# Kernel optimization log

Measured on AMD Instinct MI355X. Metric: run time of the kernel, lower is better.

## Reference

```python
import jax, jax.numpy as jnp
import numpy as np

EPS = 1e-6
NORM_FACTOR = 1000.0  # self.normalization_factor, aggregation 'sum'

# ---- Lorentz manifold (curvature -1, hyperboloid <x,x>_L = -1) ----

def _linner(x, y):
    # Lorentz inner product, keepdim on last axis
    return -x[..., :1] * y[..., :1] + jnp.sum(x[..., 1:] * y[..., 1:], axis=-1, keepdims=True)

def _proj_tan0(u):
    return jnp.concatenate([jnp.zeros_like(u[..., :1]), u[..., 1:]], axis=-1)

def _expmap0(u):
    sp = u[..., 1:]
    n = jnp.sqrt(jnp.clip(jnp.sum(sp * sp, axis=-1, keepdims=True), EPS))
    return jnp.concatenate([jnp.cosh(n), jnp.sinh(n) / n * sp], axis=-1)

def _logmap0(x):
    x0 = jnp.clip(x[..., :1], 1.0 + EPS)
    d = jnp.arccosh(x0)
    sp = x[..., 1:] * (d / jnp.sqrt(x0 * x0 - 1.0))
    return jnp.concatenate([jnp.zeros_like(x0), sp], axis=-1)

def _dist(x, y):
    return jnp.arccosh(jnp.clip(-_linner(x, y), 1.0 + EPS))

def _logmap(x, y):
    alpha = jnp.clip(-_linner(x, y), 1.0 + EPS)
    u = y - alpha * x                      # y + <x,y>_L x
    return jnp.arccosh(alpha) * u / jnp.sqrt(alpha * alpha - 1.0)

def _expmap(x, u):
    n = jnp.sqrt(jnp.clip(_linner(u, u), EPS))
    return jnp.cosh(n) * x + jnp.sinh(n) / n * u

def _proju(x, u):
    return u + _linner(x, u) * x

def _transp0(y, v):
    # parallel transport from origin o=(1,0,...,0) to y
    coef = _linner(y, v) / (1.0 + y[..., :1])
    oy = jnp.concatenate([y[..., :1] + 1.0, y[..., 1:]], axis=-1)
    return v + coef * oy

def _layernorm(x, g, b, eps=1e-5):
    m = jnp.mean(x, axis=-1, keepdims=True)
    v = jnp.mean((x - m) ** 2, axis=-1, keepdims=True)
    return (x - m) / jnp.sqrt(v + eps) * g + b


def setup_inputs() -> dict:
    N, E, D, ED = 10000, 320000, 128, 2
    key = jax.random.key(0)
    ks = jax.random.split(key, 10)
    # nodes on the hyperboloid: expmap0 of a small tangent vector
    h_tan = 0.02 * jax.random.normal(ks[0], (N, D), dtype=jnp.float32)
    h = _expmap0(_proj_tan0(h_tan))
    edge_attr = jax.random.normal(ks[1], (E, ED), dtype=jnp.float32)
    row = jax.random.randint(ks[2], (E,), 0, N, dtype=jnp.int32)
    col = jax.random.randint(ks[3], (E,), 0, N, dtype=jnp.int32)
    node_mask = jnp.ones((N, 1), dtype=jnp.float32)
    edge_mask = jnp.ones((E, 1), dtype=jnp.float32)
    s = 1.0 / np.sqrt(D)
    W = s * jax.random.normal(ks[4], (D, D), dtype=jnp.float32)
    bias = 0.0 * jax.random.normal(ks[5], (1, D), dtype=jnp.float32)  # init.constant_(bias, 0)
    att_in = 2 * D + ED + 1  # x_row, x_col, edge_attr + geodesic
    att_w1 = (1.0 / np.sqrt(att_in)) * jax.random.normal(ks[6], (att_in, D), dtype=jnp.float32)
    att_b1 = jnp.zeros((D,), dtype=jnp.float32)
    att_w2 = s * jax.random.normal(ks[7], (D, 1), dtype=jnp.float32)
    att_b2 = jnp.zeros((1,), dtype=jnp.float32)
    ln_gamma = jnp.ones((D - 1,), dtype=jnp.float32)
    ln_beta = jnp.zeros((D - 1,), dtype=jnp.float32)
    return {"h": h, "edge_attr": edge_attr, "row": row, "col": col,
            "node_mask": node_mask, "edge_mask": edge_mask, "W": W, "bias": bias,
            "att_w1": att_w1, "att_b1": att_b1, "att_w2": att_w2, "att_b2": att_b2,
            "ln_gamma": ln_gamma, "ln_beta": ln_beta}


def reference(h, edge_attr, row, col, node_mask, edge_mask, W, bias,
              att_w1, att_b1, att_w2, att_b2, ln_gamma, ln_beta):
    N = h.shape[0]
    # ---- HypLinear ----
    xt = _logmap0(h) @ W                  # Linear(in,out,bias=False)
    x = _expmap0(_proj_tan0(xt))
    b = _transp0(x, _proj_tan0(bias))
    x = _expmap(x, b)
    # ---- HypAgg ----
    x_tan = _logmap0(x)
    xr, xc = x[row], x[col]
    geo = _dist(xr, xc)                   # [E,1]
    att_in = jnp.concatenate([x_tan[row], x_tan[col], edge_attr, geo], axis=-1)
    hid = jax.nn.silu(att_in @ att_w1 + att_b1)
    att = jax.nn.sigmoid(hid @ att_w2 + att_b2) * edge_mask   # [E,1]
    loc = _logmap(xr, xc)                 # [E,D]
    agg = jax.ops.segment_sum(loc * att, row, num_segments=N) / NORM_FACTOR
    x = _expmap(x, _proju(x, agg))
    # ---- HNorm (Lorentz: LN on spatial components only) ----
    ht = _logmap0(x)
    sp = _layernorm(ht[..., 1:], ln_gamma, ln_beta)
    x = _expmap0(jnp.concatenate([ht[..., :1], sp], axis=-1))
    # ---- HypAct (manifold_out = Lorentz as well) ----
    xt = _proj_tan0(jax.nn.silu(_logmap0(x)))
    return _expmap0(xt)
```

## Files before the change

kernel.cpp:

```cpp
#include <hip/hip_runtime.h>
#include <math.h>

#define D 128
#define NPB 8
#define EPS1 (1.0f + 1e-6f)

__device__ __forceinline__ float sum16(float v) {
#pragma unroll
    for (int o = 8; o; o >>= 1) v += __shfl_xor(v, o, 64);
    return v;
}

__device__ __forceinline__ float facosh(float a) {
    return __logf(a + sqrtf(fmaxf(a * a - 1.0f, 0.0f)));
}

__device__ __forceinline__ void unpack8(const float4& a, const float4& b,
                                        float* d) {
    d[0] = a.x; d[1] = a.y; d[2] = a.z; d[3] = a.w;
    d[4] = b.x; d[5] = b.y; d[6] = b.z; d[7] = b.w;
}

__device__ __forceinline__ void bsum8(float* v, float (*wred)[NPB], int lane,
                                      int wid) {
    __syncthreads();
#pragma unroll
    for (int o = 32; o; o >>= 1)
#pragma unroll
        for (int n = 0; n < NPB; n++) v[n] += __shfl_xor(v[n], o, 64);
    if (lane == 0)
#pragma unroll
        for (int n = 0; n < NPB; n++) wred[wid][n] = v[n];
    __syncthreads();
#pragma unroll
    for (int n = 0; n < NPB; n++) v[n] = wred[0][n] + wred[1][n];
}

__global__ __launch_bounds__(128) void node_pre8(
    const float* __restrict__ h, const float* __restrict__ W,
    const float* __restrict__ bias, const float* __restrict__ att_w1,
    const float* __restrict__ att_b1, float* __restrict__ XQ,
    float* __restrict__ P_out, const int* __restrict__ row,
    int* __restrict__ cnt, int N, int E) {
    int i0 = blockIdx.x * NPB;
    int j = threadIdx.x, lane = j & 63, wid = j >> 6;
    __shared__ __align__(16) float t8[NPB][D];
    __shared__ float wred[2][NPB];

    float hj[NPB];
#pragma unroll
    for (int n = 0; n < NPB; n++) {
        hj[n] = (i0 + n < N) ? h[(size_t)(i0 + n) * D + j] : 0.0f;
        t8[n][j] = hj[n];
    }
    __syncthreads();
    float tj[NPB];
#pragma unroll
    for (int n = 0; n < NPB; n++) {
        float h0 = fmaxf(t8[n][0], EPS1);
        float fac = facosh(h0) * rsqrtf(h0 * h0 - 1.0f);
        tj[n] = (j == 0) ? 0.0f : hj[n] * fac;
    }
    __syncthreads();
#pragma unroll
    for (int n = 0; n < NPB; n++) t8[n][j] = tj[n];
    __syncthreads();

    float xt[NPB];
#pragma unroll
    for (int n = 0; n < NPB; n++) xt[n] = 0.0f;
    for (int k0 = 0; k0 < D; k0 += 4) {
        float w0 = W[(k0 + 0) * D + j], w1 = W[(k0 + 1) * D + j];
        float w2 = W[(k0 + 2) * D + j], w3 = W[(k0 + 3) * D + j];
#pragma unroll
        for (int n = 0; n < NPB; n++) {
            float4 tv = *(const float4*)&t8[n][k0];
            xt[n] = fmaf(tv.x, w0,
                         fmaf(tv.y, w1, fmaf(tv.z, w2, fmaf(tv.w, w3, xt[n]))));
        }
    }
    if (j == 0)
#pragma unroll
        for (int n = 0; n < NPB; n++) xt[n] = 0.0f;

    float v8[NPB];
#pragma unroll
    for (int n = 0; n < NPB; n++) v8[n] = xt[n] * xt[n];
    bsum8(v8, wred, lane, wid);
    float xj[NPB];
#pragma unroll
    for (int n = 0; n < NPB; n++) {
        float nn = sqrtf(fmaxf(v8[n], 1e-6f));
        float e = __expf(nn), ei = __fdividef(1.0f, e);
        float ch = 0.5f * (e + ei), sh = 0.5f * (e - ei);
        xj[n] = (j == 0) ? ch : __fdividef(sh, nn) * xt[n];
    }

    float vj = (j == 0) ? 0.0f : bias[j];
#pragma unroll
    for (int n = 0; n < NPB; n++) v8[n] = xj[n] * vj;
    bsum8(v8, wred, lane, wid);
    __syncthreads();
#pragma unroll
    for (int n = 0; n < NPB; n++) t8[n][j] = xj[n];
    __syncthreads();
    float bj[NPB];
#pragma unroll
    for (int n = 0; n < NPB; n++) {
        float X0 = t8[n][0];
        float coef = __fdividef(v8[n], 1.0f + X0);
        bj[n] = vj + coef * ((j == 0) ? (X0 + 1.0f) : xj[n]);
    }
#pragma unroll
    for (int n = 0; n < NPB; n++)
        v8[n] = (j == 0) ? -bj[n] * bj[n] : bj[n] * bj[n];
    bsum8(v8, wred, lane, wid);
    float xnj[NPB];
#pragma unroll
    for (int n = 0; n < NPB; n++) {
        float nb = sqrtf(fmaxf(v8[n], 1e-6f));
        float e = __expf(nb), ei = __fdividef(1.0f, e);
        float ch = 0.5f * (e + ei), sh = 0.5f * (e - ei);
        xnj[n] = ch * xj[n] + __fdividef(sh, nb) * bj[n];
        if (i0 + n < N) XQ[(size_t)(i0 + n) * 256 + j] = xnj[n];
    }

    __syncthreads();
#pragma unroll
    for (int n = 0; n < NPB; n++) t8[n][j] = xnj[n];
    __syncthreads();
    float xtj[NPB];
#pragma unroll
    for (int n = 0; n < NPB; n++) {
        float Y0 = fmaxf(t8[n][0], EPS1);
        float f = facosh(Y0) * rsqrtf(Y0 * Y0 - 1.0f);
        xtj[n] = (j == 0) ? 0.0f : xnj[n] * f;
    }
    __syncthreads();
#pragma unroll
    for (int n = 0; n < NPB; n++) t8[n][j] = xtj[n];
    __syncthreads();

    float p[NPB], q[NPB];
    float b1 = att_b1[j];
#pragma unroll
    for (int n = 0; n < NPB; n++) {
        p[n] = b1;
        q[n] = 0.0f;
    }
    for (int k0 = 0; k0 < D; k0 += 4) {
        float a0 = att_w1[(k0 + 0) * D + j], a1 = att_w1[(k0 + 1) * D + j];
        float a2 = att_w1[(k0 + 2) * D + j], a3 = att_w1[(k0 + 3) * D + j];
        float c0 = att_w1[(D + k0 + 0) * D + j], c1 = att_w1[(D + k0 + 1) * D + j];
        float c2 = att_w1[(D + k0 + 2) * D + j], c3 = att_w1[(D + k0 + 3) * D + j];
#pragma unroll
        for (int n = 0; n < NPB; n++) {
            float4 tv = *(const float4*)&t8[n][k0];
            p[n] = fmaf(tv.x, a0,
                        fmaf(tv.y, a1, fmaf(tv.z, a2, fmaf(tv.w, a3, p[n]))));
            q[n] = fmaf(tv.x, c0,
                        fmaf(tv.y, c1, fmaf(tv.z, c2, fmaf(tv.w, c3, q[n]))));
        }
    }
#pragma unroll
    for (int n = 0; n < NPB; n++)
        if (i0 + n < N) {
            P_out[(size_t)(i0 + n) * D + j] = p[n];
            XQ[(size_t)(i0 + n) * 256 + 128 + j] = q[n];
        }

    int gtid = blockIdx.x * 128 + threadIdx.x;
    int tot = gridDim.x * 128;
    for (int e2 = gtid; e2 < E; e2 += tot) atomicAdd(&cnt[row[e2]], 1);
}

__global__ __launch_bounds__(1024) void scan_kernel(const int* __restrict__ cnt,
                                                    int* __restrict__ off,
                                                    int* __restrict__ cursor,
                                                    int N) {
    __shared__ int wsum[16];
    __shared__ int carry_s;
    int tid = threadIdx.x, lane = tid & 63, wid = tid >> 6;
    if (tid == 0) carry_s = 0;
    __syncthreads();
    for (int base = 0; base < N; base += 1024) {
        int idx = base + tid;
        int v = (idx < N) ? cnt[idx] : 0;
        int orig = v;
#pragma unroll
        for (int o = 1; o < 64; o <<= 1) {
            int t = __shfl_up(v, o, 64);
            if (lane >= o) v += t;
        }
        if (lane == 63) wsum[wid] = v;
        __syncthreads();
        if (wid == 0 && lane < 16) {
            int w = wsum[lane];
#pragma unroll
            for (int o = 1; o < 16; o <<= 1) {
                int t = __shfl_up(w, o, 64);
                if (lane >= o) w += t;
            }
            wsum[lane] = w;
        }
        __syncthreads();
        int carry = carry_s;
        int wbase = (wid == 0) ? 0 : wsum[wid - 1];
        int excl = carry + wbase + v - orig;
        if (idx < N) {
            off[idx] = excl;
            cursor[idx] = excl;
        }
        __syncthreads();
        if (tid == 1023) carry_s = carry + wsum[15];
        __syncthreads();
    }
}

__global__ void scatter_kernel(const int* __restrict__ row,
                               const int* __restrict__ col,
                               const float* __restrict__ edge_attr,
                               const float* __restrict__ edge_mask,
                               int* __restrict__ cursor,
                               float4* __restrict__ rec, int E) {
    const float2* ea2 = (const float2*)edge_attr;
    for (int e = blockIdx.x * blockDim.x + threadIdx.x; e < E;
         e += gridDim.x * blockDim.x) {
        int r = row[e];
        int pos = atomicAdd(&cursor[r], 1);
        float2 a = ea2[e];
        rec[pos] = make_float4(__int_as_float(col[e]), a.x, a.y, edge_mask[e]);
    }
}

__global__ __launch_bounds__(256) void edge_agg(
    const float* __restrict__ XQ, const float* __restrict__ P,
    const float4* __restrict__ rec, const int* __restrict__ off,
    const int* __restrict__ cnt, const float* __restrict__ w1c,
    const float* __restrict__ att_w2, const float* __restrict__ att_b2,
    float* __restrict__ agg, int N) {
    int tid = threadIdx.x, lane = tid & 63;
    int sub = lane & 15, grp = lane >> 4;
    int i = blockIdx.x * 4 + (tid >> 6);
    bool valid = i < N;
    i = min(i, N - 1);
    int j8 = sub * 8, f4 = sub * 2;

    const float4* w4 = (const float4*)w1c;
    const float4* aw4 = (const float4*)att_w2;
    const float4* xq4r = (const float4*)(XQ + (size_t)i * 256);
    const float4* pr4 = (const float4*)(P + (size_t)i * D);
    float xr[8], pr[8], wa[8], wb[8], wg[8], w2v[8];
    unpack8(xq4r[f4], xq4r[f4 + 1], xr);
    unpack8(pr4[f4], pr4[f4 + 1], pr);
    unpack8(w4[f4], w4[f4 + 1], wa);
    unpack8(w4[32 + f4], w4[32 + f4 + 1], wb);
    unpack8(w4[64 + f4], w4[64 + f4 + 1], wg);
    unpack8(aw4[f4], aw4[f4 + 1], w2v);
    float b2 = att_b2[0];
    float xr0s = (sub == 0) ? -xr[0] : xr[0];

    float acc[8];
#pragma unroll
    for (int u = 0; u < 8; u++) acc[u] = 0.0f;

    int s = off[i], m = valid ? cnt[i] : 0;
    int clen = (m + 3) >> 2;
    int k0 = grp * clen;
    int k1 = min(m, k0 + clen);
    int len = k1 - k0;

    auto compute = [&](const float4& rc, const float4& g0, const float4& g1,
                       const float4& g2, const float4& g3, bool act) {
        float xc[8], qc[8];
        unpack8(g0, g1, xc);
        unpack8(g2, g3, qc);
        float lin = xr0s * xc[0];
#pragma unroll
        for (int u = 1; u < 8; u++) lin = fmaf(xr[u], xc[u], lin);
        lin = sum16(lin);
        float alpha = fmaxf(-lin, EPS1);
        float a2m = fmaxf(fmaf(alpha, alpha, -1.0f), 1e-12f);
        float rden = rsqrtf(a2m);
        float geo = __logf(fmaf(a2m, rden, alpha));
        float lp = 0.0f;
#pragma unroll
        for (int u = 0; u < 8; u++) {
            float hv = pr[u] + qc[u] +
                       fmaf(rc.y, wa[u], fmaf(rc.z, wb[u], geo * wg[u]));
            float sig = __fdividef(1.0f, 1.0f + __expf(-hv));
            lp = fmaf(hv * sig, w2v[u], lp);
        }
        float logit = sum16(lp) + b2;
        float w = act ? rc.w : 0.0f;
        float att = w * __fdividef(1.0f, 1.0f + __expf(-logit));
        float scale = att * geo * rden * 1e-3f;
#pragma unroll
        for (int u = 0; u < 8; u++)
            acc[u] = fmaf(scale, fmaf(-alpha, xr[u], xc[u]), acc[u]);
    };

    float4 rcA = make_float4(__int_as_float(0), 0.0f, 0.0f, 0.0f), rcB;
    if (len > 0) rcA = rec[s + k0];
    const float4* pA =
        (const float4*)(XQ + (size_t)__float_as_int(rcA.x) * 256);
    float4 gA0 = pA[f4], gA1 = pA[f4 + 1], gA2 = pA[32 + f4],
           gA3 = pA[32 + f4 + 1];
    float4 gB0, gB1, gB2, gB3;

    for (int t = 0; t < clen; t += 2) {
        rcB = rcA;
        if (t + 1 < len) rcB = rec[s + k0 + t + 1];
        const float4* pB =
            (const float4*)(XQ + (size_t)__float_as_int(rcB.x) * 256);
        gB0 = pB[f4]; gB1 = pB[f4 + 1]; gB2 = pB[32 + f4]; gB3 = pB[32 + f4 + 1];
        compute(rcA, gA0, gA1, gA2, gA3, t < len);
        rcA = rcB;
        if (t + 2 < len) rcA = rec[s + k0 + t + 2];
        const float4* pN =
            (const float4*)(XQ + (size_t)__float_as_int(rcA.x) * 256);
        gA0 = pN[f4]; gA1 = pN[f4 + 1]; gA2 = pN[32 + f4]; gA3 = pN[32 + f4 + 1];
        compute(rcB, gB0, gB1, gB2, gB3, t + 1 < len);
    }

#pragma unroll
    for (int u = 0; u < 8; u++) {
        acc[u] += __shfl_xor(acc[u], 16, 64);
        acc[u] += __shfl_xor(acc[u], 32, 64);
    }
    if (valid && grp == 0) {
        float4* a4 = (float4*)(agg + (size_t)i * D);
        a4[f4] = make_float4(acc[0], acc[1], acc[2], acc[3]);
        a4[f4 + 1] = make_float4(acc[4], acc[5], acc[6], acc[7]);
    }
}

__global__ __launch_bounds__(256) void node_post(
    const float* __restrict__ XQ, const float* __restrict__ agg,
    const float* __restrict__ gamma, const float* __restrict__ beta,
    float* __restrict__ out, int N) {
    int tid = threadIdx.x, lane = tid & 63;
    int sub = lane & 15;
    int i = blockIdx.x * 16 + (tid >> 4);
    bool valid = i < N;
    i = min(i, N - 1);
    int j8 = sub * 8, f4 = sub * 2;

    const float4* xq4r = (const float4*)(XQ + (size_t)i * 256);
    const float4* ag4 = (const float4*)(agg + (size_t)i * D);
    float xr[8], acc[8];
    unpack8(xq4r[f4], xq4r[f4 + 1], xr);
    unpack8(ag4[f4], ag4[f4 + 1], acc);

    float lxa_p = (sub == 0) ? -xr[0] * acc[0] : xr[0] * acc[0];
#pragma unroll
    for (int u = 1; u < 8; u++) lxa_p = fmaf(xr[u], acc[u], lxa_p);
    float lxa = sum16(lxa_p);
    float uj[8];
#pragma unroll
    for (int u = 0; u < 8; u++) uj[u] = fmaf(lxa, xr[u], acc[u]);
    float luu_p = (sub == 0) ? -uj[0] * uj[0] : uj[0] * uj[0];
#pragma unroll
    for (int u = 1; u < 8; u++) luu_p = fmaf(uj[u], uj[u], luu_p);
    float luu = sum16(luu_p);
    float nn = sqrtf(fmaxf(luu, 1e-6f));
    float e = __expf(nn), ei = __fdividef(1.0f, e);
    float ch = 0.5f * (e + ei), shv = __fdividef(0.5f * (e - ei), nn);
    float xn[8];
#pragma unroll
    for (int u = 0; u < 8; u++) xn[u] = ch * xr[u] + shv * uj[u];
    float X0 = __shfl(xn[0], lane & 48, 64);
    X0 = fmaxf(X0, EPS1);
    float fc = facosh(X0) * rsqrtf(X0 * X0 - 1.0f);
    float ht[8];
#pragma unroll
    for (int u = 0; u < 8; u++) ht[u] = xn[u] * fc;
    if (sub == 0) ht[0] = 0.0f;
    float mp = 0.0f;
#pragma unroll
    for (int u = 0; u < 8; u++) mp += ht[u];
    float mean = sum16(mp) * (1.0f / 127.0f);
    float diff[8];
#pragma unroll
    for (int u = 0; u < 8; u++) diff[u] = ht[u] - mean;
    if (sub == 0) diff[0] = 0.0f;
    float vp = 0.0f;
#pragma unroll
    for (int u = 0; u < 8; u++) vp = fmaf(diff[u], diff[u], vp);
    float var = sum16(vp) * (1.0f / 127.0f);
    float rstd = rsqrtf(var + 1e-5f);
    float sp[8];
#pragma unroll
    for (int u = 0; u < 8; u++) {
        int j = j8 + u;
        sp[u] = (j > 0) ? fmaf(diff[u] * rstd, gamma[j - 1], beta[j - 1]) : 0.0f;
    }
    float n2p = 0.0f;
#pragma unroll
    for (int u = 0; u < 8; u++) n2p = fmaf(sp[u], sp[u], n2p);
    float n2 = sqrtf(fmaxf(sum16(n2p), 1e-6f));
    e = __expf(n2);
    ei = __fdividef(1.0f, e);
    float y0 = 0.5f * (e + ei), sh2 = __fdividef(0.5f * (e - ei), n2);
    float yj[8];
#pragma unroll
    for (int u = 0; u < 8; u++) yj[u] = sh2 * sp[u];
    if (sub == 0) yj[0] = y0;
    float y0c = fmaxf(y0, EPS1);
    float f3 = facosh(y0c) * rsqrtf(y0c * y0c - 1.0f);
    float sj[8];
#pragma unroll
    for (int u = 0; u < 8; u++) {
        float lj = yj[u] * f3;
        sj[u] = __fdividef(lj, 1.0f + __expf(-lj));
    }
    if (sub == 0) sj[0] = 0.0f;
    float n3p = 0.0f;
#pragma unroll
    for (int u = 0; u < 8; u++) n3p = fmaf(sj[u], sj[u], n3p);
    float n3 = sqrtf(fmaxf(sum16(n3p), 1e-6f));
    e = __expf(n3);
    ei = __fdividef(1.0f, e);
    float o0 = 0.5f * (e + ei), sh3 = __fdividef(0.5f * (e - ei), n3);
    float ov[8];
#pragma unroll
    for (int u = 0; u < 8; u++) ov[u] = sh3 * sj[u];
    if (sub == 0) ov[0] = o0;
    if (valid) {
        float4* o4 = (float4*)(out + (size_t)i * D);
        o4[f4] = make_float4(ov[0], ov[1], ov[2], ov[3]);
        o4[f4 + 1] = make_float4(ov[4], ov[5], ov[6], ov[7]);
    }
}

extern "C" void kernel_launch(void* const* d_in, const int* in_sizes, int n_in,
                              void* d_out, int out_size, void* d_ws,
                              size_t ws_size, hipStream_t stream) {
    const float* h = (const float*)d_in[0];
    const float* edge_attr = (const float*)d_in[1];
    const int* row = (const int*)d_in[2];
    const int* col = (const int*)d_in[3];
    const float* edge_mask = (const float*)d_in[5];
    const float* W = (const float*)d_in[6];
    const float* bias = (const float*)d_in[7];
    const float* att_w1 = (const float*)d_in[8];
    const float* att_b1 = (const float*)d_in[9];
    const float* att_w2 = (const float*)d_in[10];
    const float* att_b2 = (const float*)d_in[11];
    const float* ln_g = (const float*)d_in[12];
    const float* ln_b = (const float*)d_in[13];

    int N = in_sizes[0] / D;
    int E = in_sizes[2];

    float* XQ = (float*)d_ws;
    float* Pbuf = XQ + (size_t)N * 256;
    float4* rec = (float4*)(Pbuf + (size_t)N * D);
    int* cnt = (int*)(rec + E);
    int* off = cnt + N;
    int* cur = off + N;
    float* aggb = (float*)(cur + N);

    hipMemsetAsync(cnt, 0, N * sizeof(int), stream);
    node_pre8<<<(N + NPB - 1) / NPB, 128, 0, stream>>>(
        h, W, bias, att_w1, att_b1, XQ, Pbuf, row, cnt, N, E);
    scan_kernel<<<1, 1024, 0, stream>>>(cnt, off, cur, N);
    scatter_kernel<<<640, 256, 0, stream>>>(row, col, edge_attr, edge_mask,
                                            cur, rec, E);
    edge_agg<<<(N + 3) / 4, 256, 0, stream>>>(XQ, Pbuf, rec, off, cnt,
                                              att_w1 + 256 * D, att_w2, att_b2,
                                              aggb, N);
    node_post<<<(N + 15) / 16, 256, 0, stream>>>(XQ, aggb, ln_g, ln_b,
                                                 (float*)d_out, N);
}
```

Baseline: 152.4 us.

## Split node_pre8 K-reduction across two thread halves and pair edges in edge_agg

node_pre8 now runs 256 threads per block. Each half computes partial matvec sums over half of the K dimension, and the halves combine them through shared memory, while per-node elementwise work is split four nodes per half. edge_agg processes two edges per compute step, interleaving their reductions and prefetching the next two edges' gathers, to raise ILP and hide gather latency. This adds shared memory and registers, which may reduce occupancy.

```diff
diff --git a/kernel.cpp b/kernel.cpp
--- a/kernel.cpp
+++ b/kernel.cpp
@@ -21,134 +21,148 @@
     d[4] = b.x; d[5] = b.y; d[6] = b.z; d[7] = b.w;
 }
 
-__device__ __forceinline__ void bsum8(float* v, float (*wred)[NPB], int lane,
-                                      int wid) {
+__device__ __forceinline__ void bsumH(float* v, float (*wred)[4], int lane,
+                                      int wid, int kp) {
     __syncthreads();
 #pragma unroll
     for (int o = 32; o; o >>= 1)
 #pragma unroll
-        for (int n = 0; n < NPB; n++) v[n] += __shfl_xor(v[n], o, 64);
+        for (int nl = 0; nl < 4; nl++) v[nl] += __shfl_xor(v[nl], o, 64);
     if (lane == 0)
 #pragma unroll
-        for (int n = 0; n < NPB; n++) wred[wid][n] = v[n];
-    __syncthreads();
-#pragma unroll
-    for (int n = 0; n < NPB; n++) v[n] = wred[0][n] + wred[1][n];
-}
-
-__global__ __launch_bounds__(128) void node_pre8(
+        for (int nl = 0; nl < 4; nl++) wred[wid][nl] = v[nl];
+    __syncthreads();
+#pragma unroll
+    for (int nl = 0; nl < 4; nl++)
+        v[nl] = wred[2 * kp][nl] + wred[2 * kp + 1][nl];
+}
+
+__global__ __launch_bounds__(256) void node_pre8(
     const float* __restrict__ h, const float* __restrict__ W,
     const float* __restrict__ bias, const float* __restrict__ att_w1,
     const float* __restrict__ att_b1, float* __restrict__ XQ,
     float* __restrict__ P_out, const int* __restrict__ row,
     int* __restrict__ cnt, int N, int E) {
     int i0 = blockIdx.x * NPB;
-    int j = threadIdx.x, lane = j & 63, wid = j >> 6;
+    int tid = threadIdx.x;
+    int j = tid & 127, kp = tid >> 7;
+    int lane = tid & 63, wid = tid >> 6;
+    int nbase = kp * 4;
     __shared__ __align__(16) float t8[NPB][D];
-    __shared__ float wred[2][NPB];
-
-    float hj[NPB];
-#pragma unroll
-    for (int n = 0; n < NPB; n++) {
-        hj[n] = (i0 + n < N) ? h[(size_t)(i0 + n) * D + j] : 0.0f;
-        t8[n][j] = hj[n];
-    }
-    __syncthreads();
-    float tj[NPB];
-#pragma unroll
-    for (int n = 0; n < NPB; n++) {
-        float h0 = fmaxf(t8[n][0], EPS1);
+    __shared__ float psumP[2][NPB][D];
+    __shared__ float psumQ[2][NPB][D];
+    __shared__ float wred[4][4];
+
+    float hj[4];
+#pragma unroll
+    for (int nl = 0; nl < 4; nl++) {
+        int gi = i0 + nbase + nl;
+        hj[nl] = (gi < N) ? h[(size_t)gi * D + j] : 0.0f;
+        t8[nbase + nl][j] = hj[nl];
+    }
+    __syncthreads();
+    float tj[4];
+#pragma unroll
+    for (int nl = 0; nl < 4; nl++) {
+        float h0 = fmaxf(t8[nbase + nl][0], EPS1);
         float fac = facosh(h0) * rsqrtf(h0 * h0 - 1.0f);
-        tj[n] = (j == 0) ? 0.0f : hj[n] * fac;
-    }
-    __syncthreads();
-#pragma unroll
-    for (int n = 0; n < NPB; n++) t8[n][j] = tj[n];
-    __syncthreads();
-
-    float xt[NPB];
-#pragma unroll
-    for (int n = 0; n < NPB; n++) xt[n] = 0.0f;
-    for (int k0 = 0; k0 < D; k0 += 4) {
+        tj[nl] = (j == 0) ? 0.0f : hj[nl] * fac;
+    }
+    __syncthreads();
+#pragma unroll
+    for (int nl = 0; nl < 4; nl++) t8[nbase + nl][j] = tj[nl];
+    __syncthreads();
+
+    float xtp[NPB];
+#pragma unroll
+    for (int n = 0; n < NPB; n++) xtp[n] = 0.0f;
+    int kbeg = kp * 64;
+    for (int k0 = kbeg; k0 < kbeg + 64; k0 += 4) {
         float w0 = W[(k0 + 0) * D + j], w1 = W[(k0 + 1) * D + j];
         float w2 = W[(k0 + 2) * D + j], w3 = W[(k0 + 3) * D + j];
 #pragma unroll
         for (int n = 0; n < NPB; n++) {
             float4 tv = *(const float4*)&t8[n][k0];
-            xt[n] = fmaf(tv.x, w0,
-                         fmaf(tv.y, w1, fmaf(tv.z, w2, fmaf(tv.w, w3, xt[n]))));
-        }
-    }
-    if (j == 0)
-#pragma unroll
-        for (int n = 0; n < NPB; n++) xt[n] = 0.0f;
-
-    float v8[NPB];
-#pragma unroll
-    for (int n = 0; n < NPB; n++) v8[n] = xt[n] * xt[n];
-    bsum8(v8, wred, lane, wid);
-    float xj[NPB];
-#pragma unroll
-    for (int n = 0; n < NPB; n++) {
-        float nn = sqrtf(fmaxf(v8[n], 1e-6f));
+            xtp[n] = fmaf(tv.x, w0,
+                          fmaf(tv.y, w1, fmaf(tv.z, w2, fmaf(tv.w, w3, xtp[n]))));
+        }
+    }
+#pragma unroll
+    for (int n = 0; n < NPB; n++) psumP[kp][n][j] = xtp[n];
+    __syncthreads();
+    float xt[4];
+#pragma unroll
+    for (int nl = 0; nl < 4; nl++) {
+        int n = nbase + nl;
+        xt[nl] = (j == 0) ? 0.0f : (psumP[0][n][j] + psumP[1][n][j]);
+    }
+
+    float v4[4];
+#pragma unroll
+    for (int nl = 0; nl < 4; nl++) v4[nl] = xt[nl] * xt[nl];
+    bsumH(v4, wred, lane, wid, kp);
+    float xj[4];
+#pragma unroll
+    for (int nl = 0; nl < 4; nl++) {
+        float nn = sqrtf(fmaxf(v4[nl], 1e-6f));
         float e = __expf(nn), ei = __fdividef(1.0f, e);
         float ch = 0.5f * (e + ei), sh = 0.5f * (e - ei);
-        xj[n] = (j == 0) ? ch : __fdividef(sh, nn) * xt[n];
+        xj[nl] = (j == 0) ? ch : __fdividef(sh, nn) * xt[nl];
     }
 
     float vj = (j == 0) ? 0.0f : bias[j];
 #pragma unroll
-    for (int n = 0; n < NPB; n++) v8[n] = xj[n] * vj;
-    bsum8(v8, wred, lane, wid);
-    __syncthreads();
-#pragma unroll
-    for (int n = 0; n < NPB; n++) t8[n][j] = xj[n];
-    __syncthreads();
-    float bj[NPB];
-#pragma unroll
-    for (int n = 0; n < NPB; n++) {
-        float X0 = t8[n][0];
-        float coef = __fdividef(v8[n], 1.0f + X0);
-        bj[n] = vj + coef * ((j == 0) ? (X0 + 1.0f) : xj[n]);
-    }
-#pragma unroll
-    for (int n = 0; n < NPB; n++)
-        v8[n] = (j == 0) ? -bj[n] * bj[n] : bj[n] * bj[n];
-    bsum8(v8, wred, lane, wid);
-    float xnj[NPB];
-#pragma unroll
-    for (int n = 0; n < NPB; n++) {
-        float nb = sqrtf(fmaxf(v8[n], 1e-6f));
+    for (int nl = 0; nl < 4; nl++) v4[nl] = xj[nl] * vj;
+    bsumH(v4, wred, lane, wid, kp);
+    __syncthreads();
+#pragma unroll
+    for (int nl = 0; nl < 4; nl++) t8[nbase + nl][j] = xj[nl];
+    __syncthreads();
+    float bj[4];
+#pragma unroll
+    for (int nl = 0; nl < 4; nl++) {
+        float X0 = t8[nbase + nl][0];
+        float coef = __fdividef(v4[nl], 1.0f + X0);
+        bj[nl] = vj + coef * ((j == 0) ? (X0 + 1.0f) : xj[nl]);
+    }
+#pragma unroll
+    for (int nl = 0; nl < 4; nl++)
+        v4[nl] = (j == 0) ? -bj[nl] * bj[nl] : bj[nl] * bj[nl];
+    bsumH(v4, wred, lane, wid, kp);
+    float xnj[4];
+#pragma unroll
+    for (int nl = 0; nl < 4; nl++) {
+        float nb = sqrtf(fmaxf(v4[nl], 1e-6f));
         float e = __expf(nb), ei = __fdividef(1.0f, e);
         float ch = 0.5f * (e + ei), sh = 0.5f * (e - ei);
-        xnj[n] = ch * xj[n] + __fdividef(sh, nb) * bj[n];
-        if (i0 + n < N) XQ[(size_t)(i0 + n) * 256 + j] = xnj[n];
-    }
-
-    __syncthreads();
-#pragma unroll
-    for (int n = 0; n < NPB; n++) t8[n][j] = xnj[n];
-    __syncthreads();
-    float xtj[NPB];
+        xnj[nl] = ch * xj[nl] + __fdividef(sh, nb) * bj[nl];
+        int gi = i0 + nbase + nl;
+        if (gi < N) XQ[(size_t)gi * 256 + j] = xnj[nl];
+    }
+
+    __syncthreads();
+#pragma unroll
+    for (int nl = 0; nl < 4; nl++) t8[nbase + nl][j] = xnj[nl];
+    __syncthreads();
+    float xtj[4];
+#pragma unroll
+    for (int nl = 0; nl < 4; nl++) {
+        float Y0 = fmaxf(t8[nbase + nl][0], EPS1);
+        float f = facosh(Y0) * rsqrtf(Y0 * Y0 - 1.0f);
+        xtj[nl] = (j == 0) ? 0.0f : xnj[nl] * f;
+    }
+    __syncthreads();
+#pragma unroll
+    for (int nl = 0; nl < 4; nl++) t8[nbase + nl][j] = xtj[nl];
+    __syncthreads();
+
+    float pp[NPB], qq[NPB];
 #pragma unroll
     for (int n = 0; n < NPB; n++) {
-        float Y0 = fmaxf(t8[n][0], EPS1);
-        float f = facosh(Y0) * rsqrtf(Y0 * Y0 - 1.0f);
-        xtj[n] = (j == 0) ? 0.0f : xnj[n] * f;
-    }
-    __syncthreads();
-#pragma unroll
-    for (int n = 0; n < NPB; n++) t8[n][j] = xtj[n];
-    __syncthreads();
-
-    float p[NPB], q[NPB];
-    float b1 = att_b1[j];
-#pragma unroll
-    for (int n = 0; n < NPB; n++) {
-        p[n] = b1;
-        q[n] = 0.0f;
-    }
-    for (int k0 = 0; k0 < D; k0 += 4) {
+        pp[n] = 0.0f;
+        qq[n] = 0.0f;
+    }
+    for (int k0 = kbeg; k0 < kbeg + 64; k0 += 4) {
         float a0 = att_w1[(k0 + 0) * D + j], a1 = att_w1[(k0 + 1) * D + j];
         float a2 = att_w1[(k0 + 2) * D + j], a3 = att_w1[(k0 + 3) * D + j];
         float c0 = att_w1[(D + k0 + 0) * D + j], c1 = att_w1[(D + k0 + 1) * D + j];
@@ -156,21 +170,31 @@
 #pragma unroll
         for (int n = 0; n < NPB; n++) {
             float4 tv = *(const float4*)&t8[n][k0];
-            p[n] = fmaf(tv.x, a0,
-                        fmaf(tv.y, a1, fmaf(tv.z, a2, fmaf(tv.w, a3, p[n]))));
-            q[n] = fmaf(tv.x, c0,
-                        fmaf(tv.y, c1, fmaf(tv.z, c2, fmaf(tv.w, c3, q[n]))));
-        }
-    }
-#pragma unroll
-    for (int n = 0; n < NPB; n++)
-        if (i0 + n < N) {
-            P_out[(size_t)(i0 + n) * D + j] = p[n];
-            XQ[(size_t)(i0 + n) * 256 + 128 + j] = q[n];
-        }
-
-    int gtid = blockIdx.x * 128 + threadIdx.x;
-    int tot = gridDim.x * 128;
+            pp[n] = fmaf(tv.x, a0,
+                         fmaf(tv.y, a1, fmaf(tv.z, a2, fmaf(tv.w, a3, pp[n]))));
+            qq[n] = fmaf(tv.x, c0,
+                         fmaf(tv.y, c1, fmaf(tv.z, c2, fmaf(tv.w, c3, qq[n]))));
+        }
+    }
+#pragma unroll
+    for (int n = 0; n < NPB; n++) {
+        psumP[kp][n][j] = pp[n];
+        psumQ[kp][n][j] = qq[n];
+    }
+    __syncthreads();
+    float b1 = att_b1[j];
+#pragma unroll
+    for (int nl = 0; nl < 4; nl++) {
+        int n = nbase + nl;
+        int gi = i0 + n;
+        if (gi < N) {
+            P_out[(size_t)gi * D + j] = psumP[0][n][j] + psumP[1][n][j] + b1;
+            XQ[(size_t)gi * 256 + 128 + j] = psumQ[0][n][j] + psumQ[1][n][j];
+        }
+    }
+
+    int gtid = blockIdx.x * 256 + tid;
+    int tot = gridDim.x * 256;
     for (int e2 = gtid; e2 < E; e2 += tot) atomicAdd(&cnt[row[e2]], 1);
 }
 
@@ -244,7 +268,7 @@
     int i = blockIdx.x * 4 + (tid >> 6);
     bool valid = i < N;
     i = min(i, N - 1);
-    int j8 = sub * 8, f4 = sub * 2;
+    int f4 = sub * 2;
 
     const float4* w4 = (const float4*)w1c;
     const float4* aw4 = (const float4*)att_w2;
@@ -267,60 +291,96 @@
     int s = off[i], m = valid ? cnt[i] : 0;
     int clen = (m + 3) >> 2;
     int k0 = grp * clen;
-    int k1 = min(m, k0 + clen);
-    int len = k1 - k0;
-
-    auto compute = [&](const float4& rc, const float4& g0, const float4& g1,
-                       const float4& g2, const float4& g3, bool act) {
-        float xc[8], qc[8];
-        unpack8(g0, g1, xc);
-        unpack8(g2, g3, qc);
-        float lin = xr0s * xc[0];
-#pragma unroll
-        for (int u = 1; u < 8; u++) lin = fmaf(xr[u], xc[u], lin);
-        lin = sum16(lin);
-        float alpha = fmaxf(-lin, EPS1);
-        float a2m = fmaxf(fmaf(alpha, alpha, -1.0f), 1e-12f);
-        float rden = rsqrtf(a2m);
-        float geo = __logf(fmaf(a2m, rden, alpha));
-        float lp = 0.0f;
+    int len = min(m, k0 + clen) - k0;
+
+    auto compute2 = [&](const float4& rc1, const float4& a0, const float4& a1,
+                        const float4& a2, const float4& a3, bool act1,
+                        const float4& rc2, const float4& b0, const float4& b1,
+                        const float4& b2q, const float4& b3, bool act2) {
+        float xc1[8], qc1[8], xc2[8], qc2[8];
+        unpack8(a0, a1, xc1);
+        unpack8(a2, a3, qc1);
+        unpack8(b0, b1, xc2);
+        unpack8(b2q, b3, qc2);
+        float lin1 = xr0s * xc1[0];
+        float lin2 = xr0s * xc2[0];
+#pragma unroll
+        for (int u = 1; u < 8; u++) {
+            lin1 = fmaf(xr[u], xc1[u], lin1);
+            lin2 = fmaf(xr[u], xc2[u], lin2);
+        }
+#pragma unroll
+        for (int o = 8; o; o >>= 1) {
+            lin1 += __shfl_xor(lin1, o, 64);
+            lin2 += __shfl_xor(lin2, o, 64);
+        }
+        float alpha1 = fmaxf(-lin1, EPS1);
+        float alpha2 = fmaxf(-lin2, EPS1);
+        float a2m1 = fmaxf(fmaf(alpha1, alpha1, -1.0f), 1e-12f);
+        float a2m2 = fmaxf(fmaf(alpha2, alpha2, -1.0f), 1e-12f);
+        float rden1 = rsqrtf(a2m1);
+        float rden2 = rsqrtf(a2m2);
+        float geo1 = __logf(fmaf(a2m1, rden1, alpha1));
+        float geo2 = __logf(fmaf(a2m2, rden2, alpha2));
+        float lp1 = 0.0f, lp2 = 0.0f;
 #pragma unroll
         for (int u = 0; u < 8; u++) {
-            float hv = pr[u] + qc[u] +
-                       fmaf(rc.y, wa[u], fmaf(rc.z, wb[u], geo * wg[u]));
-            float sig = __fdividef(1.0f, 1.0f + __expf(-hv));
-            lp = fmaf(hv * sig, w2v[u], lp);
-        }
-        float logit = sum16(lp) + b2;
-        float w = act ? rc.w : 0.0f;
-        float att = w * __fdividef(1.0f, 1.0f + __expf(-logit));
-        float scale = att * geo * rden * 1e-3f;
-#pragma unroll
-        for (int u = 0; u < 8; u++)
-            acc[u] = fmaf(scale, fmaf(-alpha, xr[u], xc[u]), acc[u]);
+            float hv1 = pr[u] + qc1[u] +
+                        fmaf(rc1.y, wa[u], fmaf(rc1.z, wb[u], geo1 * wg[u]));
+            float hv2 = pr[u] + qc2[u] +
+                        fmaf(rc2.y, wa[u], fmaf(rc2.z, wb[u], geo2 * wg[u]));
+            float sg1 = __fdividef(1.0f, 1.0f + __expf(-hv1));
+            float sg2 = __fdividef(1.0f, 1.0f + __expf(-hv2));
+            lp1 = fmaf(hv1 * sg1, w2v[u], lp1);
+            lp2 = fmaf(hv2 * sg2, w2v[u], lp2);
+        }
+#pragma unroll
+        for (int o = 8; o; o >>= 1) {
+            lp1 += __shfl_xor(lp1, o, 64);
+            lp2 += __shfl_xor(lp2, o, 64);
+        }
+        float w1 = act1 ? rc1.w : 0.0f;
+        float w2 = act2 ? rc2.w : 0.0f;
+        float att1 = w1 * __fdividef(1.0f, 1.0f + __expf(-(lp1 + b2)));
+        float att2 = w2 * __fdividef(1.0f, 1.0f + __expf(-(lp2 + b2)));
+        float sc1 = att1 * geo1 * rden1 * 1e-3f;
+        float sc2 = att2 * geo2 * rden2 * 1e-3f;
+#pragma unroll
+        for (int u = 0; u < 8; u++) {
+            acc[u] = fmaf(sc1, fmaf(-alpha1, xr[u], xc1[u]), acc[u]);
+            acc[u] = fmaf(sc2, fmaf(-alpha2, xr[u], xc2[u]), acc[u]);
+        }
     };
 
-    float4 rcA = make_float4(__int_as_float(0), 0.0f, 0.0f, 0.0f), rcB;
+    float4 z = make_float4(__int_as_float(0), 0.0f, 0.0f, 0.0f);
+    float4 rcA = z, rcB = z, rcC, rcD;
     if (len > 0) rcA = rec[s + k0];
-    const float4* pA =
-        (const float4*)(XQ + (size_t)__float_as_int(rcA.x) * 256);
+    if (len > 1) rcB = rec[s + k0 + 1];
+    const float4* pA = (const float4*)(XQ + (size_t)__float_as_int(rcA.x) * 256);
+    const float4* pB = (const float4*)(XQ + (size_t)__float_as_int(rcB.x) * 256);
     float4 gA0 = pA[f4], gA1 = pA[f4 + 1], gA2 = pA[32 + f4],
            gA3 = pA[32 + f4 + 1];
-    float4 gB0, gB1, gB2, gB3;
+    float4 gB0 = pB[f4], gB1 = pB[f4 + 1], gB2 = pB[32 + f4],
+           gB3 = pB[32 + f4 + 1];
 
     for (int t = 0; t < clen; t += 2) {
-        rcB = rcA;
-        if (t + 1 < len) rcB = rec[s + k0 + t + 1];
-        const float4* pB =
-            (const float4*)(XQ + (size_t)__float_as_int(rcB.x) * 256);
-        gB0 = pB[f4]; gB1 = pB[f4 + 1]; gB2 = pB[32 + f4]; gB3 = pB[32 + f4 + 1];
-        compute(rcA, gA0, gA1, gA2, gA3, t < len);
-        rcA = rcB;
-        if (t + 2 < len) rcA = rec[s + k0 + t + 2];
-        const float4* pN =
-            (const float4*)(XQ + (size_t)__float_as_int(rcA.x) * 256);
-        gA0 = pN[f4]; gA1 = pN[f4 + 1]; gA2 = pN[32 + f4]; gA3 = pN[32 + f4 + 1];
-        compute(rcB, gB0, gB1, gB2, gB3, t + 1 < len);
+        rcC = rcA;
+        if (t + 2 < len) rcC = rec[s + k0 + t + 2];
+        rcD = rcB;
+        if (t + 3 < len) rcD = rec[s + k0 + t + 3];
+        const float4* pC =
+            (const float4*)(XQ + (size_t)__float_as_int(rcC.x) * 256);
+        const float4* pD =
+            (const float4*)(XQ + (size_t)__float_as_int(rcD.x) * 256);
+        float4 gC0 = pC[f4], gC1 = pC[f4 + 1], gC2 = pC[32 + f4],
+               gC3 = pC[32 + f4 + 1];
+        float4 gD0 = pD[f4], gD1 = pD[f4 + 1], gD2 = pD[32 + f4],
+               gD3 = pD[32 + f4 + 1];
+        compute2(rcA, gA0, gA1, gA2, gA3, t < len, rcB, gB0, gB1, gB2, gB3,
+                 t + 1 < len);
+        rcA = rcC; rcB = rcD;
+        gA0 = gC0; gA1 = gC1; gA2 = gC2; gA3 = gC3;
+        gB0 = gD0; gB1 = gD1; gB2 = gD2; gB3 = gD3;
     }
 
 #pragma unroll
@@ -462,7 +522,7 @@
     float* aggb = (float*)(cur + N);
 
     hipMemsetAsync(cnt, 0, N * sizeof(int), stream);
-    node_pre8<<<(N + NPB - 1) / NPB, 128, 0, stream>>>(
+    node_pre8<<<(N + NPB - 1) / NPB, 256, 0, stream>>>(
         h, W, bias, att_w1, att_b1, XQ, Pbuf, row, cnt, N, E);
     scan_kernel<<<1, 1024, 0, stream>>>(cnt, off, cur, N);
     scatter_kernel<<<640, 256, 0, stream>>>(row, col, edge_attr, edge_mask,
```

Result: no change. 153.7 us (+0.9%).
